# Kernel optimization log

Measured on AMD Instinct MI355X. Metric: run time of the kernel, lower is better.

Reference implementation:

```python
import jax, jax.numpy as jnp
import numpy as np


def _grid_sample_3d(vol, grid):
    """Trilinear 3D grid_sample, zero padding, align_corners=False (torch default).

    vol:  [B, C, D, H, W]
    grid: [B, P, 3] normalized coords in [-1, 1]; grid[...,0]->W axis,
          grid[...,1]->H axis, grid[...,2]->D axis (torch convention).
    returns [B, C, P]
    """
    B, C, D, H, W = vol.shape
    x = (grid[..., 0] + 1.0) * (W * 0.5) - 0.5
    y = (grid[..., 1] + 1.0) * (H * 0.5) - 0.5
    z = (grid[..., 2] + 1.0) * (D * 0.5) - 0.5
    x0, y0, z0 = jnp.floor(x), jnp.floor(y), jnp.floor(z)
    gather = jax.vmap(lambda v, zz, yy, xx: v[:, zz, yy, xx])  # per-batch gather -> [C, P]
    out = jnp.zeros((B, C, x.shape[1]), vol.dtype)
    for dz in (0.0, 1.0):
        for dy in (0.0, 1.0):
            for dx in (0.0, 1.0):
                xi, yi, zi = x0 + dx, y0 + dy, z0 + dz
                w = (1.0 - jnp.abs(x - xi)) * (1.0 - jnp.abs(y - yi)) * (1.0 - jnp.abs(z - zi))
                valid = (xi >= 0) & (xi < W) & (yi >= 0) & (yi < H) & (zi >= 0) & (zi < D)
                xc = jnp.clip(xi, 0, W - 1).astype(jnp.int32)
                yc = jnp.clip(yi, 0, H - 1).astype(jnp.int32)
                zc = jnp.clip(zi, 0, D - 1).astype(jnp.int32)
                vals = gather(vol, zc, yc, xc)  # [B, C, P]
                out = out + vals * jnp.where(valid, w, 0.0)[:, None, :]
    return out


def _offset_grid(xs, A, Wk):
    """xs: [N,3] sample points; A: [N,3,3]; Wk: [3,K] offset weights.
    Returns [N, K, 3] grid coords ordered (z_feat, y_feat, x_feat) as in the torch code."""
    off = jnp.einsum('nij,jk->nik', A, Wk)  # bmm with repeated weight -> [N,3,K]
    xf = xs[:, 2:3] + off[:, 0, :]
    yf = xs[:, 1:2] + off[:, 1, :]
    zf = xs[:, 0:1] + off[:, 2, :]
    return jnp.stack([zf, yf, xf], axis=-1)


def setup_inputs() -> dict:
    key = jax.random.key(0)
    k1, k2, k3, k4 = jax.random.split(key, 4)
    B, C, D, H, W = 2, 16, 96, 96, 96
    Feats, K = 512, 1024
    inp = jax.random.normal(k1, (B, C, D, H, W), jnp.float32)
    xyz_sample = jax.random.uniform(k2, (B, Feats, 3), jnp.float32, -1.0, 1.0)
    A = jax.random.normal(k3, (B * Feats, 3, 3), jnp.float32) * 0.1
    weight = jax.random.normal(k4, (6, K), jnp.float32) * 0.05  # xyz_off.weight
    return {"input": inp, "xyz_sample": xyz_sample, "A": A, "weight": weight}


def reference(input, xyz_sample, A, weight):
    B, Feats, _ = xyz_sample.shape
    C = input.shape[1]
    K = weight.shape[1]  # 1024
    xs = xyz_sample.reshape(B * Feats, 3)
    g1 = _offset_grid(xs, A, weight[:3]).reshape(B, Feats * K, 3)
    g2 = _offset_grid(xs, A, weight[3:]).reshape(B, Feats * K, 3)
    feats = _grid_sample_3d(input, g1) - _grid_sample_3d(input, g2)  # [B, C, Feats*K]
    return feats.reshape(B, C * Feats, K)
```

## Files before the change

### kernel.cpp

```cpp
#include <hip/hip_runtime.h>


#define NB 2
#define NC 16
#define NS 96
#define NS3 (NS * NS * NS)
#define FEATS 512
#define NK 1024
#define PASSES 8

#define RVOX 8

__device__ __forceinline__ int stage_addr(int xg, int yg, int zg, int h) {
  int v = (zg << 6) + (yg << 3) + xg;
  int sw1 = (yg ^ (xg >> 1)) & 1;
  int sw2 = (h ^ zg) & 1;
  return (v << 6) | (sw1 << 5) | (sw2 << 4);
}

__device__ __forceinline__ unsigned int bfround(float f) {
  unsigned int u = __float_as_uint(f);
  return (u + 0x7fffu + ((u >> 16) & 1u)) >> 16;
}

#define BLO(v) __uint_as_float((v) << 16)
#define BHI(v) __uint_as_float((v) & 0xffff0000u)

__device__ __forceinline__ void tri_duo(
    const float* __restrict__ vol, size_t cbase,
    const unsigned char* __restrict__ stage, int duo,
    int ox0, int oy0, int oz0,
    float x, float y, float z, float sgn, float acc[8]) {
  float fx0 = floorf(x), fy0 = floorf(y), fz0 = floorf(z);
  int ix0 = (int)fx0, iy0 = (int)fy0, iz0 = (int)fz0;
  float tx = x - fx0, ty = y - fy0, tz = z - fz0;
  float wxa[2] = {1.0f - tx, tx};
  float wya[2] = {1.0f - ty, ty};
  float wza[2] = {1.0f - tz, tz};

  int lx0 = ix0 - ox0, ly0 = iy0 - oy0, lz0 = iz0 - oz0;
  bool fast = ((unsigned)lx0 < 7u) & ((unsigned)ly0 < 7u) & ((unsigned)lz0 < 7u);

  if (__builtin_expect(fast, 1)) {
#pragma unroll
    for (int dz = 0; dz < 2; dz++) {
      float wz = sgn * wza[dz];
      int vz = lz0 + dz;
#pragma unroll
      for (int dy = 0; dy < 2; dy++) {
        float wzy = wz * wya[dy];
        int vy = ly0 + dy;
#pragma unroll
        for (int dx = 0; dx < 2; dx++) {
          float w = wzy * wxa[dx];
          int vx = lx0 + dx;
          uint4 u = *(const uint4*)(stage + stage_addr(vx, vy, vz, duo));
          acc[0] += w * BLO(u.x);
          acc[1] += w * BHI(u.x);
          acc[2] += w * BLO(u.y);
          acc[3] += w * BHI(u.y);
          acc[4] += w * BLO(u.z);
          acc[5] += w * BHI(u.z);
          acc[6] += w * BLO(u.w);
          acc[7] += w * BHI(u.w);
        }
      }
    }
  } else {
#pragma unroll
    for (int dz = 0; dz < 2; dz++) {
      int zc = iz0 + dz;
      if ((unsigned)zc >= (unsigned)NS) continue;
#pragma unroll
      for (int dy = 0; dy < 2; dy++) {
        int yc = iy0 + dy;
        if ((unsigned)yc >= (unsigned)NS) continue;
        float wzy = sgn * wza[dz] * wya[dy];
#pragma unroll
        for (int dx = 0; dx < 2; dx++) {
          int xc = ix0 + dx;
          if ((unsigned)xc >= (unsigned)NS) continue;
          float w = wzy * wxa[dx];
          const float* p = vol + cbase + (((size_t)zc * NS + yc) * NS + xc);
#pragma unroll
          for (int c = 0; c < 8; c++)
            acc[c] += w * p[(size_t)c * NS3];
        }
      }
    }
  }
}

__global__ __launch_bounds__(256) void sample_fused(
    const float* __restrict__ vol, const float* __restrict__ xyz,
    const float* __restrict__ A, const float* __restrict__ weight,
    float* __restrict__ out) {
  __shared__ __align__(128) unsigned char stage[RVOX * RVOX * RVOX * 64];

  int n = blockIdx.x;
  int b = n >> 9;
  int f = n & 511;
  int tid = threadIdx.x;

  const float* Xn = xyz + (size_t)n * 3;
  float bx = (Xn[0] + 1.0f) * 48.0f - 0.5f;
  float by = (Xn[1] + 1.0f) * 48.0f - 0.5f;
  float bz = (Xn[2] + 1.0f) * 48.0f - 0.5f;
  int ox0 = (int)floorf(bx) - 3;
  int oy0 = (int)floorf(by) - 3;
  int oz0 = (int)floorf(bz) - 3;

  int duo = tid & 1;
  int ksub = tid >> 1;

  const float* An = A + (size_t)n * 9;
  float a00 = An[0], a01 = An[1], a02 = An[2];
  float a10 = An[3], a11 = An[4], a12 = An[5];
  float a20 = An[6], a21 = An[7], a22 = An[8];

  size_t vb = (size_t)b * NC * NS3;
#pragma unroll
  for (int j = 0; j < 4; j++) {
    int w = tid + 256 * j;
    int half = w & 1;
    int v = w >> 1;
    int xg = v & 7, yg = (v >> 3) & 7, zg = v >> 6;
    int xc = ox0 + xg, yc = oy0 + yg, zc = oz0 + zg;
    uint4 r = make_uint4(0u, 0u, 0u, 0u);
    if (((unsigned)xc < (unsigned)NS) & ((unsigned)yc < (unsigned)NS) &
        ((unsigned)zc < (unsigned)NS)) {
      const float* p = vol + vb + (size_t)(half * 8) * NS3 +
                       (((size_t)zc * NS + yc) * NS + xc);
      float f0 = p[0];
      float f1 = p[NS3];
      float f2 = p[2 * NS3];
      float f3 = p[3 * NS3];
      float f4 = p[4 * NS3];
      float f5 = p[5 * NS3];
      float f6 = p[6 * NS3];
      float f7 = p[7 * NS3];
      r.x = bfround(f0) | (bfround(f1) << 16);
      r.y = bfround(f2) | (bfround(f3) << 16);
      r.z = bfround(f4) | (bfround(f5) << 16);
      r.w = bfround(f6) | (bfround(f7) << 16);
    }
    *(uint4*)(stage + stage_addr(xg, yg, zg, half)) = r;
  }
  __syncthreads();

  size_t cbase = ((size_t)b * NC + duo * 8) * NS3;
  size_t obase = (size_t)b * (NC * FEATS * NK) +
                 (size_t)(duo * 8) * (FEATS * NK) + (size_t)f * NK;

  float wc[6], wn[6];
#pragma unroll
  for (int q = 0; q < 6; q++) wc[q] = weight[q * NK + ksub];

  for (int pass = 0; pass < PASSES; pass++) {
    int kl = pass * 128 + ksub;
    if (pass < PASSES - 1) {
#pragma unroll
      for (int q = 0; q < 6; q++) wn[q] = weight[q * NK + kl + 128];
    }

    float acc[8] = {0.0f, 0.0f, 0.0f, 0.0f, 0.0f, 0.0f, 0.0f, 0.0f};

    {
      float oz = a00 * wc[0] + a01 * wc[1] + a02 * wc[2];
      float oy = a10 * wc[0] + a11 * wc[1] + a12 * wc[2];
      float ox = a20 * wc[0] + a21 * wc[1] + a22 * wc[2];
      tri_duo(vol, cbase, stage, duo, ox0, oy0, oz0, bx + ox * 48.0f,
              by + oy * 48.0f, bz + oz * 48.0f, 1.0f, acc);
    }
    {
      float oz = a00 * wc[3] + a01 * wc[4] + a02 * wc[5];
      float oy = a10 * wc[3] + a11 * wc[4] + a12 * wc[5];
      float ox = a20 * wc[3] + a21 * wc[4] + a22 * wc[5];
      tri_duo(vol, cbase, stage, duo, ox0, oy0, oz0, bx + ox * 48.0f,
              by + oy * 48.0f, bz + oz * 48.0f, -1.0f, acc);
    }

    size_t o = obase + kl;
#pragma unroll
    for (int c = 0; c < 8; c++)
      out[o + (size_t)c * (FEATS * NK)] = acc[c];

#pragma unroll
    for (int q = 0; q < 6; q++) wc[q] = wn[q];
  }
}

extern "C" void kernel_launch(void* const* d_in, const int* in_sizes, int n_in,
                              void* d_out, int out_size, void* d_ws,
                              size_t ws_size, hipStream_t stream) {
  const float* vol    = (const float*)d_in[0];
  const float* xyz    = (const float*)d_in[1];
  const float* A      = (const float*)d_in[2];
  const float* weight = (const float*)d_in[3];
  float* out = (float*)d_out;

  sample_fused<<<NB * FEATS, 256, 0, stream>>>(vol, xyz, A, weight, out);
}
```

Measured before the change: 204.0 us.

## Compact LDS staging layout and batch all corner loads before accumulation

Packs each staged voxel into 32 bytes instead of 64, using a new swizzle, which halves the shared-memory tile per block. Adds a minimum-blocks hint to the launch bounds. Moves the fast-path check outside the two samples and issues all 16 LDS corner loads up front, then does the weighted accumulation. This raises occupancy and memory-level parallelism, at the cost of more live registers and a shared fast/slow branch: if either sample falls outside the tile, both samples take the slow global-memory path.

```diff
diff --git a/kernel.cpp b/kernel.cpp
--- a/kernel.cpp
+++ b/kernel.cpp
@@ -13,9 +13,8 @@
 
 __device__ __forceinline__ int stage_addr(int xg, int yg, int zg, int h) {
   int v = (zg << 6) + (yg << 3) + xg;
-  int sw1 = (yg ^ (xg >> 1)) & 1;
-  int sw2 = (h ^ zg) & 1;
-  return (v << 6) | (sw1 << 5) | (sw2 << 4);
+  v ^= (yg & 1) << 1;
+  return (v << 5) | (((h ^ zg) & 1) << 4);
 }
 
 __device__ __forceinline__ unsigned int bfround(float f) {
@@ -26,10 +25,19 @@
 #define BLO(v) __uint_as_float((v) << 16)
 #define BHI(v) __uint_as_float((v) & 0xffff0000u)
 
-__device__ __forceinline__ void tri_duo(
+__device__ __forceinline__ void acc8(const uint4& u, float wt, float acc[8]) {
+  acc[0] += wt * BLO(u.x);
+  acc[1] += wt * BHI(u.x);
+  acc[2] += wt * BLO(u.y);
+  acc[3] += wt * BHI(u.y);
+  acc[4] += wt * BLO(u.z);
+  acc[5] += wt * BHI(u.z);
+  acc[6] += wt * BLO(u.w);
+  acc[7] += wt * BHI(u.w);
+}
+
+__device__ __forceinline__ void tri_slow(
     const float* __restrict__ vol, size_t cbase,
-    const unsigned char* __restrict__ stage, int duo,
-    int ox0, int oy0, int oz0,
     float x, float y, float z, float sgn, float acc[8]) {
   float fx0 = floorf(x), fy0 = floorf(y), fz0 = floorf(z);
   int ix0 = (int)fx0, iy0 = (int)fy0, iz0 = (int)fz0;
@@ -37,65 +45,34 @@
   float wxa[2] = {1.0f - tx, tx};
   float wya[2] = {1.0f - ty, ty};
   float wza[2] = {1.0f - tz, tz};
-
-  int lx0 = ix0 - ox0, ly0 = iy0 - oy0, lz0 = iz0 - oz0;
-  bool fast = ((unsigned)lx0 < 7u) & ((unsigned)ly0 < 7u) & ((unsigned)lz0 < 7u);
-
-  if (__builtin_expect(fast, 1)) {
-#pragma unroll
-    for (int dz = 0; dz < 2; dz++) {
-      float wz = sgn * wza[dz];
-      int vz = lz0 + dz;
-#pragma unroll
-      for (int dy = 0; dy < 2; dy++) {
-        float wzy = wz * wya[dy];
-        int vy = ly0 + dy;
-#pragma unroll
-        for (int dx = 0; dx < 2; dx++) {
-          float w = wzy * wxa[dx];
-          int vx = lx0 + dx;
-          uint4 u = *(const uint4*)(stage + stage_addr(vx, vy, vz, duo));
-          acc[0] += w * BLO(u.x);
-          acc[1] += w * BHI(u.x);
-          acc[2] += w * BLO(u.y);
-          acc[3] += w * BHI(u.y);
-          acc[4] += w * BLO(u.z);
-          acc[5] += w * BHI(u.z);
-          acc[6] += w * BLO(u.w);
-          acc[7] += w * BHI(u.w);
-        }
-      }
-    }
-  } else {
-#pragma unroll
-    for (int dz = 0; dz < 2; dz++) {
-      int zc = iz0 + dz;
-      if ((unsigned)zc >= (unsigned)NS) continue;
-#pragma unroll
-      for (int dy = 0; dy < 2; dy++) {
-        int yc = iy0 + dy;
-        if ((unsigned)yc >= (unsigned)NS) continue;
-        float wzy = sgn * wza[dz] * wya[dy];
-#pragma unroll
-        for (int dx = 0; dx < 2; dx++) {
-          int xc = ix0 + dx;
-          if ((unsigned)xc >= (unsigned)NS) continue;
-          float w = wzy * wxa[dx];
-          const float* p = vol + cbase + (((size_t)zc * NS + yc) * NS + xc);
-#pragma unroll
-          for (int c = 0; c < 8; c++)
-            acc[c] += w * p[(size_t)c * NS3];
-        }
+#pragma unroll
+  for (int dz = 0; dz < 2; dz++) {
+    int zc = iz0 + dz;
+    if ((unsigned)zc >= (unsigned)NS) continue;
+#pragma unroll
+    for (int dy = 0; dy < 2; dy++) {
+      int yc = iy0 + dy;
+      if ((unsigned)yc >= (unsigned)NS) continue;
+      float wzy = sgn * wza[dz] * wya[dy];
+#pragma unroll
+      for (int dx = 0; dx < 2; dx++) {
+        int xc = ix0 + dx;
+        if ((unsigned)xc >= (unsigned)NS) continue;
+        float w = wzy * wxa[dx];
+        const float* p = vol + cbase + (((size_t)zc * NS + yc) * NS + xc);
+#pragma unroll
+        for (int c = 0; c < 8; c++)
+          acc[c] += w * p[(size_t)c * NS3];
       }
     }
   }
 }
 
-__global__ __launch_bounds__(256) void sample_fused(
+__global__ __launch_bounds__(256, 4) void sample_fused(
     const float* __restrict__ vol, const float* __restrict__ xyz,
     const float* __restrict__ A, const float* __restrict__ weight,
     float* __restrict__ out) {
-  __shared__ __align__(128) unsigned char stage[RVOX * RVOX * RVOX * 64];
+  __shared__ __align__(128) unsigned char stage[RVOX * RVOX * RVOX * 32];
 
   int n = blockIdx.x;
   int b = n >> 9;
@@ -165,19 +142,69 @@
 
     float acc[8] = {0.0f, 0.0f, 0.0f, 0.0f, 0.0f, 0.0f, 0.0f, 0.0f};
 
-    {
-      float oz = a00 * wc[0] + a01 * wc[1] + a02 * wc[2];
-      float oy = a10 * wc[0] + a11 * wc[1] + a12 * wc[2];
-      float ox = a20 * wc[0] + a21 * wc[1] + a22 * wc[2];
-      tri_duo(vol, cbase, stage, duo, ox0, oy0, oz0, bx + ox * 48.0f,
-              by + oy * 48.0f, bz + oz * 48.0f, 1.0f, acc);
-    }
-    {
-      float oz = a00 * wc[3] + a01 * wc[4] + a02 * wc[5];
-      float oy = a10 * wc[3] + a11 * wc[4] + a12 * wc[5];
-      float ox = a20 * wc[3] + a21 * wc[4] + a22 * wc[5];
-      tri_duo(vol, cbase, stage, duo, ox0, oy0, oz0, bx + ox * 48.0f,
-              by + oy * 48.0f, bz + oz * 48.0f, -1.0f, acc);
+    float oz1 = a00 * wc[0] + a01 * wc[1] + a02 * wc[2];
+    float oy1 = a10 * wc[0] + a11 * wc[1] + a12 * wc[2];
+    float ox1 = a20 * wc[0] + a21 * wc[1] + a22 * wc[2];
+    float oz2 = a00 * wc[3] + a01 * wc[4] + a02 * wc[5];
+    float oy2 = a10 * wc[3] + a11 * wc[4] + a12 * wc[5];
+    float ox2 = a20 * wc[3] + a21 * wc[4] + a22 * wc[5];
+    float x1 = bx + ox1 * 48.0f, y1 = by + oy1 * 48.0f, z1 = bz + oz1 * 48.0f;
+    float x2 = bx + ox2 * 48.0f, y2 = by + oy2 * 48.0f, z2 = bz + oz2 * 48.0f;
+
+    float fx1 = floorf(x1), fy1 = floorf(y1), fz1 = floorf(z1);
+    float fx2 = floorf(x2), fy2 = floorf(y2), fz2 = floorf(z2);
+    int lx1 = (int)fx1 - ox0, ly1 = (int)fy1 - oy0, lz1 = (int)fz1 - oz0;
+    int lx2 = (int)fx2 - ox0, ly2 = (int)fy2 - oy0, lz2 = (int)fz2 - oz0;
+    bool fast =
+        ((unsigned)lx1 < 7u) & ((unsigned)ly1 < 7u) & ((unsigned)lz1 < 7u) &
+        ((unsigned)lx2 < 7u) & ((unsigned)ly2 < 7u) & ((unsigned)lz2 < 7u);
+
+    if (__builtin_expect(fast, 1)) {
+      uint4 G1[8], G2[8];
+#pragma unroll
+      for (int i = 0; i < 8; i++) {
+        int dx = i & 1, dy = (i >> 1) & 1, dz = i >> 2;
+        G1[i] = *(const uint4*)(stage +
+                                stage_addr(lx1 + dx, ly1 + dy, lz1 + dz, duo));
+      }
+#pragma unroll
+      for (int i = 0; i < 8; i++) {
+        int dx = i & 1, dy = (i >> 1) & 1, dz = i >> 2;
+        G2[i] = *(const uint4*)(stage +
+                                stage_addr(lx2 + dx, ly2 + dy, lz2 + dz, duo));
+      }
+
+      float tx1 = x1 - fx1, ty1 = y1 - fy1, tz1 = z1 - fz1;
+      float tx2 = x2 - fx2, ty2 = y2 - fy2, tz2 = z2 - fz2;
+      float W1[8], W2[8];
+      {
+        float w00 = (1.0f - tz1) * (1.0f - ty1);
+        float w01 = (1.0f - tz1) * ty1;
+        float w10 = tz1 * (1.0f - ty1);
+        float w11 = tz1 * ty1;
+        W1[0] = w00 * (1.0f - tx1); W1[1] = w00 * tx1;
+        W1[2] = w01 * (1.0f - tx1); W1[3] = w01 * tx1;
+        W1[4] = w10 * (1.0f - tx1); W1[5] = w10 * tx1;
+        W1[6] = w11 * (1.0f - tx1); W1[7] = w11 * tx1;
+      }
+      {
+        float w00 = -(1.0f - tz2) * (1.0f - ty2);
+        float w01 = -(1.0f - tz2) * ty2;
+        float w10 = -tz2 * (1.0f - ty2);
+        float w11 = -tz2 * ty2;
+        W2[0] = w00 * (1.0f - tx2); W2[1] = w00 * tx2;
+        W2[2] = w01 * (1.0f - tx2); W2[3] = w01 * tx2;
+        W2[4] = w10 * (1.0f - tx2); W2[5] = w10 * tx2;
+        W2[6] = w11 * (1.0f - tx2); W2[7] = w11 * tx2;
+      }
+
+#pragma unroll
+      for (int i = 0; i < 8; i++) acc8(G1[i], W1[i], acc);
+#pragma unroll
+      for (int i = 0; i < 8; i++) acc8(G2[i], W2[i], acc);
+    } else {
+      tri_slow(vol, cbase, x1, y1, z1, 1.0f, acc);
+      tri_slow(vol, cbase, x2, y2, z2, -1.0f, acc);
     }
 
     size_t o = obase + kl;
```

Result: no change. 204.1 us (+0.0%).
